# Performance work log

Hardware: AMD Instinct MI355X
Metric: run time of the kernel (lower is better)

## Reference

```python
import jax, jax.numpy as jnp
import numpy as np
import math

D_MODEL = 1024
N_HEADS = 16
D_HEAD = 64
VOCAB = 32000
MAX_SEQ = 2048
PAD_TOKEN = 0
EPS = 1e-5
NEG = -1000000000.0


def layer_norm(x, g, b):
    m = jnp.mean(x, axis=-1, keepdims=True)
    v = jnp.mean(jnp.square(x - m), axis=-1, keepdims=True)
    return (x - m) * jax.lax.rsqrt(v + EPS) * g + b


def setup_inputs() -> dict:
    key = jax.random.key(0)
    ks = jax.random.split(key, 12)
    s = 0.02
    inp = {
        "tokens": jax.random.randint(ks[0], (2, 2048), 0, VOCAB, dtype=jnp.int64)
            if jax.config.jax_enable_x64 else jax.random.randint(ks[0], (2, 2048), 0, VOCAB, dtype=jnp.int32),
        "emb": jax.random.normal(ks[1], (VOCAB, D_MODEL), jnp.float32) * s,
        "pos_emb": jax.random.normal(ks[2], (MAX_SEQ, D_MODEL), jnp.float32) * s,
        "ln1_g": jnp.ones((D_MODEL,), jnp.float32), "ln1_b": jnp.zeros((D_MODEL,), jnp.float32),
        "ln2_g": jnp.ones((D_MODEL,), jnp.float32), "ln2_b": jnp.zeros((D_MODEL,), jnp.float32),
        "ln3_g": jnp.ones((D_MODEL,), jnp.float32), "ln3_b": jnp.zeros((D_MODEL,), jnp.float32),
        "Wq": jax.random.normal(ks[3], (D_MODEL, N_HEADS * D_HEAD), jnp.float32) * s,
        "bq": jnp.zeros((N_HEADS * D_HEAD,), jnp.float32),
        "Wk": jax.random.normal(ks[4], (D_MODEL, N_HEADS * D_HEAD), jnp.float32) * s,
        "bk": jnp.zeros((N_HEADS * D_HEAD,), jnp.float32),
        "Wv": jax.random.normal(ks[5], (D_MODEL, N_HEADS * D_HEAD), jnp.float32) * s,
        "bv": jnp.zeros((N_HEADS * D_HEAD,), jnp.float32),
        "Wo": jax.random.normal(ks[6], (N_HEADS * D_HEAD, D_MODEL), jnp.float32) * s,
        "bo": jnp.zeros((D_MODEL,), jnp.float32),
        "W1": jax.random.normal(ks[7], (D_MODEL, 4 * D_MODEL), jnp.float32) * s,
        "b1": jnp.zeros((4 * D_MODEL,), jnp.float32),
        "W2": jax.random.normal(ks[8], (4 * D_MODEL, D_MODEL), jnp.float32) * s,
        "b2": jnp.zeros((D_MODEL,), jnp.float32),
    }
    return inp


def reference(tokens, emb, pos_emb, ln1_g, ln1_b, ln2_g, ln2_b, ln3_g, ln3_b,
              Wq, bq, Wk, bk, Wv, bv, Wo, bo, W1, b1, W2, b2):
    b, s = tokens.shape
    # embedding + learned positional embedding
    x = emb[tokens] + pos_emb[jnp.arange(s)][None, :, :]  # [b,s,d]
    x = layer_norm(x, ln1_g, ln1_b)
    Q = (x @ Wq + bq).reshape(b, s, N_HEADS, D_HEAD).transpose(0, 2, 1, 3)  # [b,n,s,d]
    K = (x @ Wk + bk).reshape(b, s, N_HEADS, D_HEAD).transpose(0, 2, 1, 3)
    V = (x @ Wv + bv).reshape(b, s, N_HEADS, D_HEAD).transpose(0, 2, 1, 3)
    logits = jnp.einsum('bnsd,bntd->bnst', Q, K) / math.sqrt(D_HEAD)  # [b,n,s,s]
    causal = jnp.triu(jnp.full((s, s), NEG, jnp.float32), k=1)
    pad_mask = jnp.where(tokens == PAD_TOKEN, NEG, 0.0)  # keys masked: [b,s]
    logits = logits + causal[None, None, :, :] + pad_mask[:, None, None, :]
    probs = jax.nn.softmax(logits, axis=-1)
    attn = jnp.einsum('bnst,bntd->bnsd', probs, V)
    attn = attn.transpose(0, 2, 1, 3).reshape(b, s, N_HEADS * D_HEAD)
    attn_out = attn @ Wo + bo
    x = x + layer_norm(attn_out, ln2_g, ln2_b)
    h = jax.nn.gelu(layer_norm(x, ln3_g, ln3_b) @ W1 + b1, approximate=False)
    x = x + (h @ W2 + b2)
    return x
```

## Files before the change

kernel.cpp:

```cpp
#include <hip/hip_runtime.h>
#include <cstdint>
#include <cstddef>


#define SEQ     2048
#define NTOK    4096
#define DMODEL  1024
#define NHEAD   16
#define DHEAD   64
#define MASKV   (-30.0f)
#define LN_EPS  1e-5f

typedef __bf16 bf16_t;
typedef __bf16 bf16x8 __attribute__((ext_vector_type(8)));
typedef float  f32x4  __attribute__((ext_vector_type(4)));

#define MFMA_BF16(a,b,c) __builtin_amdgcn_mfma_f32_16x16x32_bf16((a),(b),(c),0,0,0)

__device__ __forceinline__ void gload_lds16(const void* g, void* l) {
  __builtin_amdgcn_global_load_lds(
      (__attribute__((address_space(1))) void*)(g),
      (__attribute__((address_space(3))) void*)(l), 16, 0, 0);
}

__global__ __launch_bounds__(256)
void wtrans_kernel(const float* __restrict__ W, bf16_t* __restrict__ WT,
                   int K, int N) {
  __shared__ float tile[64][65];
  const int n0 = blockIdx.x * 64, k0 = blockIdx.y * 64;
  const int c = threadIdx.x & 63, rb = threadIdx.x >> 6;
#pragma unroll
  for (int i = 0; i < 16; ++i) {
    int r = i * 4 + rb;
    tile[r][c] = W[(size_t)(k0 + r) * N + n0 + c];
  }
  __syncthreads();
#pragma unroll
  for (int i = 0; i < 16; ++i) {
    int r = i * 4 + rb;
    WT[(size_t)(n0 + r) * K + k0 + c] = (bf16_t)tile[c][r];
  }
}

__global__ __launch_bounds__(256)
void pack_bias_kernel(const float* __restrict__ bq, const float* __restrict__ bk,
                      const float* __restrict__ bv, float* __restrict__ o) {
  int i = blockIdx.x * 256 + threadIdx.x;
  if (i < 1024) { o[i] = bq[i]; o[1024 + i] = bk[i]; o[2048 + i] = bv[i]; }
}

__global__ __launch_bounds__(256)
void ln1_kernel(const int* __restrict__ tokens, const float* __restrict__ emb,
                const float* __restrict__ pos, const float* __restrict__ g,
                const float* __restrict__ bb, float* __restrict__ xln,
                bf16_t* __restrict__ xlnb) {
  __shared__ float red[8];
  const int t = blockIdx.x;
  const int s = t & (SEQ - 1);
  const int tok = tokens[t];
  const int d0 = threadIdx.x * 4;
  const int w = threadIdx.x >> 6, lane = threadIdx.x & 63;

  float4 e  = *(const float4*)(emb + (size_t)tok * DMODEL + d0);
  float4 pp = *(const float4*)(pos + (size_t)s   * DMODEL + d0);
  float x0 = e.x + pp.x, x1 = e.y + pp.y, x2v = e.z + pp.z, x3v = e.w + pp.w;
  float s1 = x0 + x1 + x2v + x3v;
  float s2 = x0*x0 + x1*x1 + x2v*x2v + x3v*x3v;
#pragma unroll
  for (int o = 32; o >= 1; o >>= 1) { s1 += __shfl_xor(s1, o); s2 += __shfl_xor(s2, o); }
  if (lane == 0) { red[w] = s1; red[4 + w] = s2; }
  __syncthreads();
  s1 = red[0] + red[1] + red[2] + red[3];
  s2 = red[4] + red[5] + red[6] + red[7];
  float mean = s1 * (1.0f / DMODEL);
  float var  = s2 * (1.0f / DMODEL) - mean * mean;
  float inv  = rsqrtf(var + LN_EPS);
  float4 gv = *(const float4*)(g + d0);
  float4 bv = *(const float4*)(bb + d0);
  float y0 = (x0  - mean) * inv * gv.x + bv.x;
  float y1 = (x1  - mean) * inv * gv.y + bv.y;
  float y2 = (x2v - mean) * inv * gv.z + bv.z;
  float y3 = (x3v - mean) * inv * gv.w + bv.w;
  *(float4*)(xln + (size_t)t * DMODEL + d0) = make_float4(y0, y1, y2, y3);
  union { ushort4 u; bf16_t b[4]; } cv;
  cv.b[0] = (bf16_t)y0; cv.b[1] = (bf16_t)y1; cv.b[2] = (bf16_t)y2; cv.b[3] = (bf16_t)y3;
  *(ushort4*)(xlnb + (size_t)t * DMODEL + d0) = cv.u;
}

__global__ __launch_bounds__(256)
void ln23_kernel(const float* __restrict__ ao, const float* __restrict__ xln,
                 const float* __restrict__ g2, const float* __restrict__ bb2,
                 const float* __restrict__ g3, const float* __restrict__ bb3,
                 float* __restrict__ x2o, bf16_t* __restrict__ x3b) {
  __shared__ float red[8];
  const int t = blockIdx.x;
  const int d0 = threadIdx.x * 4;
  const int w = threadIdx.x >> 6, lane = threadIdx.x & 63;

  float4 a = *(const float4*)(ao + (size_t)t * DMODEL + d0);
  float s1 = a.x + a.y + a.z + a.w;
  float s2 = a.x*a.x + a.y*a.y + a.z*a.z + a.w*a.w;
#pragma unroll
  for (int o = 32; o >= 1; o >>= 1) { s1 += __shfl_xor(s1, o); s2 += __shfl_xor(s2, o); }
  if (lane == 0) { red[w] = s1; red[4 + w] = s2; }
  __syncthreads();
  s1 = red[0] + red[1] + red[2] + red[3];
  s2 = red[4] + red[5] + red[6] + red[7];
  float mean = s1 * (1.0f / DMODEL);
  float var  = s2 * (1.0f / DMODEL) - mean * mean;
  float inv  = rsqrtf(var + LN_EPS);
  float4 gv = *(const float4*)(g2 + d0);
  float4 bv = *(const float4*)(bb2 + d0);
  float4 xv = *(const float4*)(xln + (size_t)t * DMODEL + d0);
  float y0 = xv.x + (a.x - mean) * inv * gv.x + bv.x;
  float y1 = xv.y + (a.y - mean) * inv * gv.y + bv.y;
  float y2 = xv.z + (a.z - mean) * inv * gv.z + bv.z;
  float y3 = xv.w + (a.w - mean) * inv * gv.w + bv.w;
  *(float4*)(x2o + (size_t)t * DMODEL + d0) = make_float4(y0, y1, y2, y3);

  float t1 = y0 + y1 + y2 + y3;
  float t2 = y0*y0 + y1*y1 + y2*y2 + y3*y3;
#pragma unroll
  for (int o = 32; o >= 1; o >>= 1) { t1 += __shfl_xor(t1, o); t2 += __shfl_xor(t2, o); }
  __syncthreads();
  if (lane == 0) { red[w] = t1; red[4 + w] = t2; }
  __syncthreads();
  t1 = red[0] + red[1] + red[2] + red[3];
  t2 = red[4] + red[5] + red[6] + red[7];
  float mean2 = t1 * (1.0f / DMODEL);
  float var2  = t2 * (1.0f / DMODEL) - mean2 * mean2;
  float inv2  = rsqrtf(var2 + LN_EPS);
  float4 gv3 = *(const float4*)(g3 + d0);
  float4 bv3 = *(const float4*)(bb3 + d0);
  union { ushort4 u; bf16_t b[4]; } cv;
  cv.b[0] = (bf16_t)((y0 - mean2) * inv2 * gv3.x + bv3.x);
  cv.b[1] = (bf16_t)((y1 - mean2) * inv2 * gv3.y + bv3.y);
  cv.b[2] = (bf16_t)((y2 - mean2) * inv2 * gv3.z + bv3.z);
  cv.b[3] = (bf16_t)((y3 - mean2) * inv2 * gv3.w + bv3.w);
  *(ushort4*)(x3b + (size_t)t * DMODEL + d0) = cv.u;
}

constexpr int EPI_BF16 = 0, EPI_F32 = 1, EPI_GELU = 2, EPI_RES = 3;

template <int EPI>
__global__ __launch_bounds__(256, 2)
void gemm_bt(const bf16_t* __restrict__ A, const bf16_t* __restrict__ B,
             const float* __restrict__ bias, const float* __restrict__ res,
             bf16_t* __restrict__ obf, float* __restrict__ of32,
             int M, int N, int K) {
  __shared__ __attribute__((aligned(16))) bf16_t As[128 * 64];
  __shared__ __attribute__((aligned(16))) bf16_t Bs[128 * 64];
  const int tid = threadIdx.x;
  const int w = tid >> 6, lane = tid & 63;
  const int quad = lane >> 4, l16 = lane & 15;
  const int m0 = blockIdx.x * 128, n0 = blockIdx.y * 128;
  const int wm = (w >> 1) * 64, wn = (w & 1) * 64;
  const size_t Kz = (size_t)K;

  f32x4 acc[4][4] = {};

  const bf16_t* Ag = A + (size_t)(m0 + w * 32 + (lane >> 3)) * Kz + (lane & 7) * 8;
  const bf16_t* Bg = B + (size_t)(n0 + w * 32 + (lane >> 3)) * Kz + (lane & 7) * 8;
  bf16_t* Asw = &As[(w * 32) * 64];
  bf16_t* Bsw = &Bs[(w * 32) * 64];

  for (int k0 = 0; k0 < K; k0 += 64) {
#pragma unroll
    for (int i = 0; i < 4; ++i) {
      gload_lds16(Ag + (size_t)i * 8 * Kz + k0, Asw + i * 8 * 64);
      gload_lds16(Bg + (size_t)i * 8 * Kz + k0, Bsw + i * 8 * 64);
    }
    __syncthreads();
#pragma unroll
    for (int kc = 0; kc < 2; ++kc) {
      bf16x8 af[4], bfr[4];
#pragma unroll
      for (int i = 0; i < 4; ++i) {
        af[i]  = *(const bf16x8*)&As[(wm + i * 16 + l16) * 64 + kc * 32 + quad * 8];
        bfr[i] = *(const bf16x8*)&Bs[(wn + i * 16 + l16) * 64 + kc * 32 + quad * 8];
      }
#pragma unroll
      for (int mi = 0; mi < 4; ++mi)
#pragma unroll
        for (int ni = 0; ni < 4; ++ni)
          acc[mi][ni] = MFMA_BF16(af[mi], bfr[ni], acc[mi][ni]);
    }
    __syncthreads();
  }

#pragma unroll
  for (int ni = 0; ni < 4; ++ni) {
    const int col = n0 + wn + ni * 16 + l16;
    const float bv = bias[col];
#pragma unroll
    for (int mi = 0; mi < 4; ++mi) {
#pragma unroll
      for (int r = 0; r < 4; ++r) {
        const int row = m0 + wm + mi * 16 + quad * 4 + r;
        float v = acc[mi][ni][r] + bv;
        if constexpr (EPI == EPI_GELU)
          v = 0.5f * v * (1.0f + erff(v * 0.70710678118654752f));
        if constexpr (EPI == EPI_RES)
          v += res[(size_t)row * N + col];
        if constexpr (EPI == EPI_BF16 || EPI == EPI_GELU)
          obf[(size_t)row * N + col] = (bf16_t)v;
        else
          of32[(size_t)row * N + col] = v;
      }
    }
  }
}

__global__ __launch_bounds__(256)
void vtrans_kernel(const bf16_t* __restrict__ qkv, bf16_t* __restrict__ Vt) {
  __shared__ bf16_t tile[64][72];
  const int bh = blockIdx.y;
  const int b = bh >> 4, h = bh & 15;
  const int s0 = blockIdx.x * 64;
  const int c = threadIdx.x & 63, rb = threadIdx.x >> 6;
#pragma unroll
  for (int i = 0; i < 16; ++i) {
    int r = i * 4 + rb;
    tile[r][c] = qkv[(size_t)(b * SEQ + s0 + r) * 3072 + 2048 + h * 64 + c];
  }
  __syncthreads();
#pragma unroll
  for (int i = 0; i < 16; ++i) {
    int r = i * 4 + rb;
    Vt[((size_t)bh * 64 + r) * SEQ + s0 + c] = tile[c][r];
  }
}

__global__ __launch_bounds__(256, 2)
void attn_kernel(const bf16_t* __restrict__ qkv, const bf16_t* __restrict__ Vt,
                 const int* __restrict__ tokens, bf16_t* __restrict__ attnb) {
  __shared__ __attribute__((aligned(16))) bf16_t Ks[128 * 64];
  __shared__ __attribute__((aligned(16))) bf16_t Vts[64 * 136];
  __shared__ __attribute__((aligned(16))) bf16_t Ps[4][32 * 136];

  const int tid = threadIdx.x;
  const int w = tid >> 6, lane = tid & 63;
  const int quad = lane >> 4, l16 = lane & 15;
  const int bh = blockIdx.x;
  const int strip = 15 - (int)blockIdx.y;
  const int b = bh >> 4, h = bh & 15;
  const int ntiles = strip + 1;
  const int qrow0 = strip * 128 + w * 32;

  const bf16_t* Kbase = qkv + (size_t)b * SEQ * 3072 + 1024 + h * 64;
  const bf16_t* Vbase = Vt + (size_t)bh * 64 * SEQ;
  const int*    tokb  = tokens + b * SEQ;
  bf16_t* Pw = Ps[w];

  const int sw_chunk = (lane & 7) ^ ((lane >> 3) & 7);
  const int xr = l16 & 7;

  bf16x8 qf[2][2];
#pragma unroll
  for (int mi = 0; mi < 2; ++mi) {
    const size_t trow = (size_t)(b * SEQ + qrow0 + mi * 16 + l16) * 3072 + h * 64;
    qf[mi][0] = *(const bf16x8*)(qkv + trow + quad * 8);
    qf[mi][1] = *(const bf16x8*)(qkv + trow + 32 + quad * 8);
  }

  bf16x8 onev;
#pragma unroll
  for (int j = 0; j < 8; ++j) onev[j] = (bf16_t)1.0f;

  f32x4 oacc[2][4] = {};
  f32x4 lacc[2] = {};

  for (int kt = 0; kt < ntiles; ++kt) {
    const int k0 = kt * 128;
    {
      const bf16_t* Kg = Kbase + (size_t)(k0 + w * 32 + (lane >> 3)) * 3072
                         + sw_chunk * 8;
      bf16_t* Kl = &Ks[(w * 32) * 64];
#pragma unroll
      for (int i = 0; i < 4; ++i)
        gload_lds16(Kg + (size_t)i * 8 * 3072, Kl + i * 8 * 64);
    }
#pragma unroll
    for (int i = 0; i < 4; ++i) {
      int idx = i * 256 + tid;
      int d = idx >> 4, c = idx & 15;
      uint4 v = *(const uint4*)(Vbase + (size_t)d * SEQ + k0 + c * 8);
      *(uint4*)&Vts[d * 136 + c * 8] = v;
    }
    __syncthreads();

    float padneg[8];
#pragma unroll
    for (int ni = 0; ni < 8; ++ni)
      padneg[ni] = (tokb[k0 + ni * 16 + l16] == 0) ? MASKV : 0.0f;

    const bool diag = (kt == ntiles - 1);

    f32x4 sc0[8] = {}, sc1[8] = {};
#pragma unroll
    for (int kc = 0; kc < 2; ++kc)
#pragma unroll
      for (int ni = 0; ni < 8; ++ni) {
        bf16x8 kf = *(const bf16x8*)&Ks[(ni * 16 + l16) * 64
                                        + ((kc * 4 + quad) ^ xr) * 8];
        sc0[ni] = MFMA_BF16(qf[0][kc], kf, sc0[ni]);
        sc1[ni] = MFMA_BF16(qf[1][kc], kf, sc1[ni]);
      }

#pragma unroll
    for (int mi = 0; mi < 2; ++mi) {
      f32x4* sc = mi ? sc1 : sc0;
      const int qg = qrow0 + mi * 16 + quad * 4;
#pragma unroll
      for (int ni = 0; ni < 8; ++ni) {
        const int key = k0 + ni * 16 + l16;
#pragma unroll
        for (int r = 0; r < 4; ++r) {
          float v = sc[ni][r] * 0.125f + padneg[ni];
          if (diag && key > qg + r) v += MASKV;
          Pw[(mi * 16 + quad * 4 + r) * 136 + ni * 16 + l16] = (bf16_t)__expf(v);
        }
      }
    }

#pragma unroll
    for (int kc2 = 0; kc2 < 4; ++kc2) {
      bf16x8 pf0 = *(const bf16x8*)&Pw[l16 * 136 + kc2 * 32 + quad * 8];
      bf16x8 pf1 = *(const bf16x8*)&Pw[(16 + l16) * 136 + kc2 * 32 + quad * 8];
      lacc[0] = MFMA_BF16(pf0, onev, lacc[0]);
      lacc[1] = MFMA_BF16(pf1, onev, lacc[1]);
#pragma unroll
      for (int nd = 0; nd < 4; ++nd) {
        bf16x8 vf = *(const bf16x8*)&Vts[(nd * 16 + l16) * 136
                                         + kc2 * 32 + quad * 8];
        oacc[0][nd] = MFMA_BF16(pf0, vf, oacc[0][nd]);
        oacc[1][nd] = MFMA_BF16(pf1, vf, oacc[1][nd]);
      }
    }
    __syncthreads();
  }

#pragma unroll
  for (int mi = 0; mi < 2; ++mi)
#pragma unroll
    for (int r = 0; r < 4; ++r) {
      const int q = qrow0 + mi * 16 + quad * 4 + r;
      const float invl = 1.0f / lacc[mi][r];
#pragma unroll
      for (int nd = 0; nd < 4; ++nd)
        attnb[(size_t)(b * SEQ + q) * DMODEL + h * 64 + nd * 16 + l16] =
            (bf16_t)(oacc[mi][nd][r] * invl);
    }
}

extern "C" void kernel_launch(void* const* d_in, const int* in_sizes, int n_in,
                              void* d_out, int out_size, void* d_ws, size_t ws_size,
                              hipStream_t stream) {
  const int*   tokens = (const int*)d_in[0];
  const float* emb    = (const float*)d_in[1];
  const float* pos    = (const float*)d_in[2];
  const float* ln1g   = (const float*)d_in[3];
  const float* ln1b   = (const float*)d_in[4];
  const float* ln2g   = (const float*)d_in[5];
  const float* ln2b   = (const float*)d_in[6];
  const float* ln3g   = (const float*)d_in[7];
  const float* ln3b   = (const float*)d_in[8];
  const float* Wq     = (const float*)d_in[9];
  const float* bq     = (const float*)d_in[10];
  const float* Wk     = (const float*)d_in[11];
  const float* bk     = (const float*)d_in[12];
  const float* Wv     = (const float*)d_in[13];
  const float* bv     = (const float*)d_in[14];
  const float* Wo     = (const float*)d_in[15];
  const float* bo     = (const float*)d_in[16];
  const float* W1     = (const float*)d_in[17];
  const float* b1     = (const float*)d_in[18];
  const float* W2     = (const float*)d_in[19];
  const float* b2     = (const float*)d_in[20];
  float* out = (float*)d_out;

  char* p = (char*)d_ws;
  auto alloc = [&](size_t bytes) {
    char* q = p; p += (bytes + 255) & ~(size_t)255; return q;
  };
  float*  x_ln   = (float*)alloc((size_t)NTOK * DMODEL * 4);
  bf16_t* x_lnb  = (bf16_t*)alloc((size_t)NTOK * DMODEL * 2);
  bf16_t* WqkvT  = (bf16_t*)alloc((size_t)3072 * 1024 * 2);
  float*  bqkv   = (float*)alloc(3072 * 4);
  bf16_t* WoT    = (bf16_t*)alloc((size_t)1024 * 1024 * 2);
  bf16_t* W1T    = (bf16_t*)alloc((size_t)4096 * 1024 * 2);
  bf16_t* W2T    = (bf16_t*)alloc((size_t)1024 * 4096 * 2);
  bf16_t* qkvb   = (bf16_t*)alloc((size_t)NTOK * 3072 * 2);
  bf16_t* Vtb    = (bf16_t*)alloc((size_t)32 * 64 * SEQ * 2);
  bf16_t* attnb  = (bf16_t*)alloc((size_t)NTOK * DMODEL * 2);
  float*  attn_o = (float*)alloc((size_t)NTOK * DMODEL * 4);
  float*  x2     = (float*)alloc((size_t)NTOK * DMODEL * 4);
  bf16_t* x3b    = (bf16_t*)alloc((size_t)NTOK * DMODEL * 2);
  bf16_t* hbuf   = (bf16_t*)alloc((size_t)NTOK * 4096 * 2);

  wtrans_kernel<<<dim3(16, 16), 256, 0, stream>>>(Wq, WqkvT,                 1024, 1024);
  wtrans_kernel<<<dim3(16, 16), 256, 0, stream>>>(Wk, WqkvT + 1024ull * 1024, 1024, 1024);
  wtrans_kernel<<<dim3(16, 16), 256, 0, stream>>>(Wv, WqkvT + 2048ull * 1024, 1024, 1024);
  wtrans_kernel<<<dim3(16, 16), 256, 0, stream>>>(Wo, WoT, 1024, 1024);
  wtrans_kernel<<<dim3(64, 16), 256, 0, stream>>>(W1, W1T, 1024, 4096);
  wtrans_kernel<<<dim3(16, 64), 256, 0, stream>>>(W2, W2T, 4096, 1024);
  pack_bias_kernel<<<4, 256, 0, stream>>>(bq, bk, bv, bqkv);

  ln1_kernel<<<NTOK, 256, 0, stream>>>(tokens, emb, pos, ln1g, ln1b, x_ln, x_lnb);

  gemm_bt<EPI_BF16><<<dim3(32, 24), 256, 0, stream>>>(
      x_lnb, WqkvT, bqkv, nullptr, qkvb, nullptr, NTOK, 3072, 1024);

  vtrans_kernel<<<dim3(32, 32), 256, 0, stream>>>(qkvb, Vtb);

  attn_kernel<<<dim3(32, 16), 256, 0, stream>>>(qkvb, Vtb, tokens, attnb);

  gemm_bt<EPI_F32><<<dim3(32, 8), 256, 0, stream>>>(
      attnb, WoT, bo, nullptr, nullptr, attn_o, NTOK, 1024, 1024);

  ln23_kernel<<<NTOK, 256, 0, stream>>>(attn_o, x_ln, ln2g, ln2b, ln3g, ln3b, x2, x3b);

  gemm_bt<EPI_GELU><<<dim3(32, 32), 256, 0, stream>>>(
      x3b, W1T, b1, nullptr, hbuf, nullptr, NTOK, 4096, 1024);

  gemm_bt<EPI_RES><<<dim3(32, 8), 256, 0, stream>>>(
      hbuf, W2T, b2, x2, nullptr, out, NTOK, 1024, 4096);

  (void)in_sizes; (void)n_in; (void)out_size; (void)ws_size;
}
```

Baseline: 562.7 us.

## Keep attention P in registers via transposed MFMA and read K/V directly

The attention kernel is restructured so S^T is computed with K as the A operand. The exponentiated scores can then be packed into bf16 MFMA operands straight from registers, with no per-wave shared-memory P buffer. K and V tiles are read directly from global memory instead of being staged through LDS, which removes the __syncthreads barriers. It also folds the 1/8 scale into Q, preloads the pad mask as the accumulator init, skips masked key chunks on the diagonal tile, and interleaves strip order to balance blocks. The risk is higher global/L2 traffic and load latency because K/V are no longer shared across the four waves through LDS.

Result: slower. 582.9 us (+3.6%).

```diff
diff --git a/kernel.cpp b/kernel.cpp
--- a/kernel.cpp
+++ b/kernel.cpp
@@ -231,29 +231,110 @@
   }
 }
 
+
+__device__ __forceinline__ unsigned pack2_bf16(float e, float o) {
+  union { bf16_t b; unsigned short s; } lo, hi;
+  lo.b = (bf16_t)e; hi.b = (bf16_t)o;
+  return (unsigned)lo.s | ((unsigned)hi.s << 16);
+}
+
+template <bool DIAG>
+__device__ __forceinline__ void attn_tile(
+    int k0, int chunkCnt, int w, int quad, int l16, int krow,
+    const bf16_t* __restrict__ Kbase, const bf16_t* __restrict__ Vbase,
+    const int* __restrict__ tokb,
+    const bf16x8 (&qf)[2][2], bf16x8 onev,
+    f32x4 (&oacc)[2][4], f32x4 (&lacc)[2]) {
+
+  f32x4 sc0[8], sc1[8];
+
+#pragma unroll
+  for (int c = 0; c < 4; ++c)
+    if (!DIAG || c < chunkCnt) {
+      int4 t0 = *(const int4*)(tokb + k0 + 32 * c + 8 * quad);
+      int4 t1 = *(const int4*)(tokb + k0 + 32 * c + 8 * quad + 4);
+      f32x4 pe, po;
+      pe[0] = (t0.x == 0) ? MASKV : 0.0f;
+      po[0] = (t0.y == 0) ? MASKV : 0.0f;
+      pe[1] = (t0.z == 0) ? MASKV : 0.0f;
+      po[1] = (t0.w == 0) ? MASKV : 0.0f;
+      pe[2] = (t1.x == 0) ? MASKV : 0.0f;
+      po[2] = (t1.y == 0) ? MASKV : 0.0f;
+      pe[3] = (t1.z == 0) ? MASKV : 0.0f;
+      po[3] = (t1.w == 0) ? MASKV : 0.0f;
+      sc0[2 * c] = pe; sc0[2 * c + 1] = po;
+      sc1[2 * c] = pe; sc1[2 * c + 1] = po;
+    }
+
+#pragma unroll
+  for (int kc = 0; kc < 2; ++kc)
+#pragma unroll
+    for (int ni = 0; ni < 8; ++ni)
+      if (!DIAG || ni < 2 * chunkCnt) {
+        bf16x8 kf = *(const bf16x8*)(Kbase
+            + (size_t)(k0 + 32 * (ni >> 1) + (ni & 1) + krow) * 3072
+            + kc * 32 + quad * 8);
+        sc0[ni] = MFMA_BF16(kf, qf[0][kc], sc0[ni]);
+        sc1[ni] = MFMA_BF16(kf, qf[1][kc], sc1[ni]);
+      }
+
+#pragma unroll
+  for (int mi = 0; mi < 2; ++mi) {
+    f32x4* sc = mi ? sc1 : sc0;
+    const int ql = w * 32 + mi * 16 + l16;
+#pragma unroll
+    for (int ni = 0; ni < 8; ++ni)
+      if (!DIAG || ni < 2 * chunkCnt) {
+#pragma unroll
+        for (int r = 0; r < 4; ++r) {
+          float v = sc[ni][r];
+          if (DIAG) {
+            int keyl = 32 * (ni >> 1) + (ni & 1) + 8 * quad + 2 * r;
+            if (keyl > ql) v += MASKV;
+          }
+          sc[ni][r] = __expf(v);
+        }
+      }
+  }
+
+#pragma unroll
+  for (int c = 0; c < 4; ++c)
+    if (!DIAG || c < chunkCnt) {
+      union { unsigned u[4]; bf16x8 v; } pb0, pb1;
+#pragma unroll
+      for (int m = 0; m < 4; ++m) {
+        pb0.u[m] = pack2_bf16(sc0[2 * c][m], sc0[2 * c + 1][m]);
+        pb1.u[m] = pack2_bf16(sc1[2 * c][m], sc1[2 * c + 1][m]);
+      }
+      lacc[0] = MFMA_BF16(onev, pb0.v, lacc[0]);
+      lacc[1] = MFMA_BF16(onev, pb1.v, lacc[1]);
+#pragma unroll
+      for (int nd = 0; nd < 4; ++nd) {
+        bf16x8 vf = *(const bf16x8*)(Vbase
+            + (size_t)(nd * 16 + l16) * SEQ + k0 + c * 32 + quad * 8);
+        oacc[0][nd] = MFMA_BF16(vf, pb0.v, oacc[0][nd]);
+        oacc[1][nd] = MFMA_BF16(vf, pb1.v, oacc[1][nd]);
+      }
+    }
+}
+
 __global__ __launch_bounds__(256, 2)
 void attn_kernel(const bf16_t* __restrict__ qkv, const bf16_t* __restrict__ Vt,
                  const int* __restrict__ tokens, bf16_t* __restrict__ attnb) {
-  __shared__ __attribute__((aligned(16))) bf16_t Ks[128 * 64];
-  __shared__ __attribute__((aligned(16))) bf16_t Vts[64 * 136];
-  __shared__ __attribute__((aligned(16))) bf16_t Ps[4][32 * 136];
-
   const int tid = threadIdx.x;
   const int w = tid >> 6, lane = tid & 63;
   const int quad = lane >> 4, l16 = lane & 15;
   const int bh = blockIdx.x;
-  const int strip = 15 - (int)blockIdx.y;
+  const int by = (int)blockIdx.y;
+  const int strip = (by < 8) ? (15 - by) : (by - 8);
   const int b = bh >> 4, h = bh & 15;
   const int ntiles = strip + 1;
   const int qrow0 = strip * 128 + w * 32;
+  const int krow = ((l16 >> 2) << 3) + ((l16 & 3) << 1);
 
   const bf16_t* Kbase = qkv + (size_t)b * SEQ * 3072 + 1024 + h * 64;
   const bf16_t* Vbase = Vt + (size_t)bh * 64 * SEQ;
   const int*    tokb  = tokens + b * SEQ;
-  bf16_t* Pw = Ps[w];
-
-  const int sw_chunk = (lane & 7) ^ ((lane >> 3) & 7);
-  const int xr = l16 & 7;
 
   bf16x8 qf[2][2];
 #pragma unroll
@@ -262,6 +343,13 @@
     qf[mi][0] = *(const bf16x8*)(qkv + trow + quad * 8);
     qf[mi][1] = *(const bf16x8*)(qkv + trow + 32 + quad * 8);
   }
+#pragma unroll
+  for (int mi = 0; mi < 2; ++mi)
+#pragma unroll
+    for (int kc = 0; kc < 2; ++kc)
+#pragma unroll
+      for (int j = 0; j < 8; ++j)
+        qf[mi][kc][j] = (bf16_t)((float)qf[mi][kc][j] * 0.125f);
 
   bf16x8 onev;
 #pragma unroll
@@ -270,87 +358,26 @@
   f32x4 oacc[2][4] = {};
   f32x4 lacc[2] = {};
 
-  for (int kt = 0; kt < ntiles; ++kt) {
-    const int k0 = kt * 128;
-    {
-      const bf16_t* Kg = Kbase + (size_t)(k0 + w * 32 + (lane >> 3)) * 3072
-                         + sw_chunk * 8;
-      bf16_t* Kl = &Ks[(w * 32) * 64];
-#pragma unroll
-      for (int i = 0; i < 4; ++i)
-        gload_lds16(Kg + (size_t)i * 8 * 3072, Kl + i * 8 * 64);
-    }
-#pragma unroll
-    for (int i = 0; i < 4; ++i) {
-      int idx = i * 256 + tid;
-      int d = idx >> 4, c = idx & 15;
-      uint4 v = *(const uint4*)(Vbase + (size_t)d * SEQ + k0 + c * 8);
-      *(uint4*)&Vts[d * 136 + c * 8] = v;
-    }
-    __syncthreads();
-
-    float padneg[8];
-#pragma unroll
-    for (int ni = 0; ni < 8; ++ni)
-      padneg[ni] = (tokb[k0 + ni * 16 + l16] == 0) ? MASKV : 0.0f;
-
-    const bool diag = (kt == ntiles - 1);
-
-    f32x4 sc0[8] = {}, sc1[8] = {};
-#pragma unroll
-    for (int kc = 0; kc < 2; ++kc)
-#pragma unroll
-      for (int ni = 0; ni < 8; ++ni) {
-        bf16x8 kf = *(const bf16x8*)&Ks[(ni * 16 + l16) * 64
-                                        + ((kc * 4 + quad) ^ xr) * 8];
-        sc0[ni] = MFMA_BF16(qf[0][kc], kf, sc0[ni]);
-        sc1[ni] = MFMA_BF16(qf[1][kc], kf, sc1[ni]);
-      }
-
-#pragma unroll
-    for (int mi = 0; mi < 2; ++mi) {
-      f32x4* sc = mi ? sc1 : sc0;
-      const int qg = qrow0 + mi * 16 + quad * 4;
-#pragma unroll
-      for (int ni = 0; ni < 8; ++ni) {
-        const int key = k0 + ni * 16 + l16;
-#pragma unroll
-        for (int r = 0; r < 4; ++r) {
-          float v = sc[ni][r] * 0.125f + padneg[ni];
-          if (diag && key > qg + r) v += MASKV;
-          Pw[(mi * 16 + quad * 4 + r) * 136 + ni * 16 + l16] = (bf16_t)__expf(v);
-        }
-      }
-    }
-
-#pragma unroll
-    for (int kc2 = 0; kc2 < 4; ++kc2) {
-      bf16x8 pf0 = *(const bf16x8*)&Pw[l16 * 136 + kc2 * 32 + quad * 8];
-      bf16x8 pf1 = *(const bf16x8*)&Pw[(16 + l16) * 136 + kc2 * 32 + quad * 8];
-      lacc[0] = MFMA_BF16(pf0, onev, lacc[0]);
-      lacc[1] = MFMA_BF16(pf1, onev, lacc[1]);
-#pragma unroll
-      for (int nd = 0; nd < 4; ++nd) {
-        bf16x8 vf = *(const bf16x8*)&Vts[(nd * 16 + l16) * 136
-                                         + kc2 * 32 + quad * 8];
-        oacc[0][nd] = MFMA_BF16(pf0, vf, oacc[0][nd]);
-        oacc[1][nd] = MFMA_BF16(pf1, vf, oacc[1][nd]);
-      }
-    }
-    __syncthreads();
-  }
-
-#pragma unroll
-  for (int mi = 0; mi < 2; ++mi)
-#pragma unroll
-    for (int r = 0; r < 4; ++r) {
-      const int q = qrow0 + mi * 16 + quad * 4 + r;
-      const float invl = 1.0f / lacc[mi][r];
-#pragma unroll
-      for (int nd = 0; nd < 4; ++nd)
-        attnb[(size_t)(b * SEQ + q) * DMODEL + h * 64 + nd * 16 + l16] =
-            (bf16_t)(oacc[mi][nd][r] * invl);
-    }
+  for (int kt = 0; kt < ntiles - 1; ++kt)
+    attn_tile<false>(kt * 128, 4, w, quad, l16, krow,
+                     Kbase, Vbase, tokb, qf, onev, oacc, lacc);
+  attn_tile<true>((ntiles - 1) * 128, w + 1, w, quad, l16, krow,
+                  Kbase, Vbase, tokb, qf, onev, oacc, lacc);
+
+#pragma unroll
+  for (int mi = 0; mi < 2; ++mi) {
+    const float invl = 1.0f / lacc[mi][0];
+    const size_t row =
+        (size_t)(b * SEQ + qrow0 + mi * 16 + l16) * DMODEL + h * 64;
+#pragma unroll
+    for (int nd = 0; nd < 4; ++nd) {
+      union { ushort4 u; bf16_t bv[4]; } cv;
+#pragma unroll
+      for (int r = 0; r < 4; ++r)
+        cv.bv[r] = (bf16_t)(oacc[mi][nd][r] * invl);
+      *(ushort4*)(attnb + row + nd * 16 + quad * 4) = cv.u;
+    }
+  }
 }
 
 extern "C" void kernel_launch(void* const* d_in, const int* in_sizes, int n_in,
```
